# Optimization experiments

Measured on AMD Instinct MI355X. Metric: run time of the kernel, lower is better.

## Reference

```python
import jax, jax.numpy as jnp
import numpy as np

K = 3          # kernel_size
P = 1          # padding
S = 1          # stride
C_IN = 64
C_OUT = 64


def unfold_patches(t, k=K, p=P, s=S):
    """Replicate-pad then extract kxk patches.
    Input  t: [B, C, H, W]
    Output  : [B, Ho, Wo, C, k*k]  matching torch unfold(2).unfold(3).permute(0,2,3,1,4,5).reshape
    (patch index varies as kh*k + kw)."""
    B, C, H, W = t.shape
    tp = jnp.pad(t, ((0, 0), (0, 0), (p, p), (p, p)), mode='edge')
    Ho = (H + 2 * p - k) // s + 1
    Wo = (W + 2 * p - k) // s + 1
    pats = [tp[:, :, a:a + (Ho - 1) * s + 1:s, b:b + (Wo - 1) * s + 1:s]
            for a in range(k) for b in range(k)]
    y = jnp.stack(pats, axis=-1)          # [B, C, Ho, Wo, k*k]
    return jnp.transpose(y, (0, 2, 3, 1, 4))  # [B, Ho, Wo, C, k*k]


def setup_inputs() -> dict:
    key = jax.random.key(0)
    k1, k2, k3, k4, k5, k6, k7 = jax.random.split(key, 7)
    B, H, W = 4, 128, 128
    feat_in = K * K * C_IN * 2      # 1152
    f1_out = K * K * C_IN           # 576
    f2_out = C_IN * C_OUT           # 4096
    lim1 = 1.0 / np.sqrt(feat_in)
    x = jax.random.normal(k1, (B, C_IN, H, W), dtype=jnp.float32)
    m = jax.random.uniform(k2, (B, C_IN, H, W), dtype=jnp.float32)
    s = jax.random.uniform(k3, (B, C_IN, H, W), dtype=jnp.float32)
    W1 = jax.random.uniform(k4, (feat_in, f1_out), minval=-lim1, maxval=lim1, dtype=jnp.float32)
    b1 = jax.random.uniform(k5, (f1_out,), minval=-lim1, maxval=lim1, dtype=jnp.float32)
    W2 = jax.random.uniform(k6, (feat_in, f2_out), minval=-lim1, maxval=lim1, dtype=jnp.float32)
    b2 = jax.random.uniform(k7, (f2_out,), minval=-lim1, maxval=lim1, dtype=jnp.float32)
    return {"x": x, "m": m, "s": s, "W1": W1, "b1": b1, "W2": W2, "b2": b2}


def reference(x, m, s, W1, b1, W2, b2):
    yp = unfold_patches(x)                              # [B,Ho,Wo,Cin,K2]
    mp = jax.lax.stop_gradient(unfold_patches(m))       # torch no_grad
    sp = jax.lax.stop_gradient(unfold_patches(s))
    B, Ho, Wo = yp.shape[:3]

    feat = jnp.concatenate([yp.reshape(B, Ho, Wo, -1),
                            mp.reshape(B, Ho, Wo, -1)], axis=-1)  # [B,Ho,Wo,2*K2*Cin]
    w1 = (feat @ W1 + b1).reshape(B, Ho, Wo, C_IN, K * K)
    w2 = (feat @ W2 + b2).reshape(B, Ho, Wo, C_IN, C_OUT)

    # y = sum_c (sum_k yp*w1) * w2
    yr = jnp.einsum('bhwck,bhwck->bhwc', yp, w1)
    y = jnp.einsum('bhwc,bhwco->bhwo', yr, w2)
    y = jnp.transpose(y, (0, 3, 1, 2))                  # [B,Cout,Ho,Wo]

    aw1 = jnp.abs(w1)
    aw2 = jnp.abs(w2)
    mr = jnp.einsum('bhwck,bhwck->bhwc', mp, aw1)
    m_y = jnp.transpose(jnp.einsum('bhwc,bhwco->bhwo', mr, aw2), (0, 3, 1, 2))
    sr = jnp.einsum('bhwck,bhwck->bhwc', sp, aw1)
    s_y = jnp.transpose(jnp.einsum('bhwc,bhwco->bhwo', sr, aw2), (0, 3, 1, 2))
    m_y = jax.lax.stop_gradient(m_y / s_y)

    return (y, m_y, jnp.ones_like(m_y))
```

## Files before the change

### kernel.cpp

```cpp
#include <hip/hip_runtime.h>
#include <stdint.h>
#include <stddef.h>


using short8   = __attribute__((ext_vector_type(8))) short;
using float4v  = __attribute__((ext_vector_type(4))) float;
using ushort4v = __attribute__((ext_vector_type(4))) unsigned short;

#define DI __device__ __forceinline__

DI unsigned short f2bf(float f) {
  union { float f; unsigned int u; } a; a.f = f;
  unsigned int r = a.u + 0x7fffu + ((a.u >> 16) & 1u);
  return (unsigned short)(r >> 16);
}
DI float bf2f(unsigned short u) {
  union { unsigned int u; float f; } a; a.u = ((unsigned int)u) << 16;
  return a.f;
}
DI void gll16(const void* g, void* l) {
  __builtin_amdgcn_global_load_lds(
      (const __attribute__((address_space(1))) unsigned int*)g,
      (__attribute__((address_space(3))) unsigned int*)l, 16, 0, 0);
}

__global__ void k_feat(const float* __restrict__ x, const float* __restrict__ m,
                       unsigned short* __restrict__ featb) {
  unsigned int v = blockIdx.x * 256u + threadIdx.x;
  unsigned int f = v * 8u;
  int pl   = (f >> 3) & 127;
  int q    = (f >> 10) & 3;
  int pblk = (f >> 12) & 511;
  int kk   = (int)(f >> 21);
  int base = kk * 32 + q * 8;
  const float* src = x;
  int jb = base;
  if (base >= 576) { src = m; jb = base - 576; }
  int p  = pblk * 128 + pl;
  int b  = p >> 14, h = (p >> 7) & 127;
  short8 o;
#pragma unroll
  for (int j = 0; j < 8; ++j) {
    int jx = jb + j;
    int c  = jx / 9;
    int t  = jx - c * 9;
    int t3 = t / 3;
    int dh = t3 - 1;
    int dw = (t - t3 * 3) - 1;
    int hh = min(max(h + dh, 0), 127);
    int ww = min(max(pl + dw, 0), 127);
    o[j] = (short)f2bf(src[(((b << 6) | c) << 14) + (hh << 7) + ww]);
  }
  *(short8*)&featb[(size_t)v * 8] = o;
}

__global__ void k_sw(const float* __restrict__ Wsrc, unsigned short* __restrict__ Wdst,
                     int ncols, int ntiles, int total, int perm) {
  int tid = blockIdx.x * 256 + threadIdx.x;
  if (tid >= total) return;
  int k = tid / ncols;
  int n = tid - k * ncols;
  int np = perm ? (((n & 63) << 6) | (n >> 6)) : n;
  int out = ((k >> 5) * ntiles + (np >> 4)) * 512 + ((k >> 3) & 3) * 128 +
            (np & 15) * 8 + (k & 7);
  Wdst[out] = f2bf(Wsrc[tid]);
}

__launch_bounds__(512, 2)
__global__ void k_gemm1(const unsigned short* __restrict__ featb,
                        const unsigned short* __restrict__ W1s,
                        const float* __restrict__ b1,
                        const float* __restrict__ x, const float* __restrict__ m,
                        const float* __restrict__ s,
                        float* __restrict__ yr, float* __restrict__ mr,
                        float* __restrict__ sr) {
  __shared__ __align__(16) unsigned short Alds[4096];
  __shared__ __align__(16) unsigned short Blds[4608];
  __shared__ __align__(16) unsigned short w1buf[128 * 152];
  const int tid = threadIdx.x;
  const int wv  = tid >> 6;
  const int l15 = tid & 15;
  const int q   = (tid >> 4) & 3;
  const int bm  = blockIdx.x, nb = blockIdx.y;

  float4v acc[9];
#pragma unroll
  for (int t = 0; t < 9; ++t) acc[t] = (float4v){0.f, 0.f, 0.f, 0.f};

  const unsigned short* Ab = featb + (size_t)bm * 4096;
  const unsigned short* Bb = W1s + (size_t)nb * 9 * 512;

  for (int kk = 0; kk < 36; ++kk) {
    __syncthreads();
    gll16(Ab + (size_t)kk * 2097152 + tid * 8, (char*)Alds + wv * 1024);
    gll16(Bb + (size_t)kk * 18432 + tid * 8, (char*)Blds + wv * 1024);
    if (tid < 64) gll16(Bb + (size_t)kk * 18432 + 4096 + tid * 8, (char*)Blds + 8192);
    __syncthreads();
    short8 af = *(const short8*)&Alds[q * 1024 + (16 * wv + l15) * 8];
#pragma unroll
    for (int t = 0; t < 9; ++t) {
      short8 bfr = *(const short8*)&Blds[t * 512 + q * 128 + l15 * 8];
      acc[t] = __builtin_amdgcn_mfma_f32_16x16x32_bf16(af, bfr, acc[t], 0, 0, 0);
    }
  }

#pragma unroll
  for (int t = 0; t < 9; ++t) {
    int col = 16 * t + l15;
    float bb = b1[nb * 144 + col];
#pragma unroll
    for (int i = 0; i < 4; ++i) {
      int plr = 16 * wv + 4 * q + i;
      w1buf[plr * 152 + col] = f2bf(acc[t][i] + bb);
    }
  }
  __syncthreads();

  const int b = bm >> 7, h = bm & 127;
#pragma unroll
  for (int ii = 0; ii < 4; ++ii) {
    int task = ii * 512 + tid;
    int p  = task >> 4;
    int cl = task & 15;
    int c  = nb * 16 + cl;
    float w1v[9];
#pragma unroll
    for (int k = 0; k < 9; ++k) w1v[k] = bf2f(w1buf[p * 152 + cl * 9 + k]);
    size_t base = (size_t)(((b << 6) | c) << 14);
    float vy = 0.f, vm = 0.f, vs = 0.f;
#pragma unroll
    for (int dh = -1; dh <= 1; ++dh) {
      int hh = min(max(h + dh, 0), 127);
#pragma unroll
      for (int dw = -1; dw <= 1; ++dw) {
        int ww = min(max(p + dw, 0), 127);
        size_t idx = base + (hh << 7) + ww;
        int k = (dh + 1) * 3 + (dw + 1);
        float wv1 = w1v[k], aw = fabsf(wv1);
        vy += x[idx] * wv1;
        vm += m[idx] * aw;
        vs += s[idx] * aw;
      }
    }
    size_t P = (size_t)bm * 128 + p;
    yr[P * 64 + c] = vy;
    mr[P * 64 + c] = vm;
    sr[P * 64 + c] = vs;
  }
}

__launch_bounds__(512, 4)
__global__ void k_gemm2(const unsigned short* __restrict__ featb,
                        const unsigned short* __restrict__ W2s,
                        const float* __restrict__ b2,
                        const float* __restrict__ yr, const float* __restrict__ mr,
                        const float* __restrict__ sr,
                        float* __restrict__ out) {
  __shared__ __align__(16) unsigned short U[3][12288];
  unsigned short* w2buf = &U[2][0];
  const int tid  = threadIdx.x;
  const int wv   = tid >> 6;
  const int lane = tid & 63;
  const int wm   = wv >> 2;
  const int wn   = wv & 3;
  const int l15  = tid & 15;
  const int q    = (tid >> 4) & 3;
  const int part = lane >> 4;
  const int bm   = blockIdx.x;
  const int rot  = (bm & 1) * 18;

  const unsigned short* Ab = featb + (size_t)bm * 4096;

  float4v acc[4][4];
#pragma unroll
  for (int r = 0; r < 4; ++r)
#pragma unroll
    for (int t = 0; t < 4; ++t) acc[r][t] = (float4v){0.f, 0.f, 0.f, 0.f};

  {
    int p0 = rot, p1 = rot + 1;
    gll16(Ab + (size_t)p0 * 2097152 + tid * 8, (char*)&U[0][0]    + wv * 1024);
    gll16(W2s + (size_t)p0 * 131072 + tid * 8, (char*)&U[0][4096] + wv * 1024);
    gll16(W2s + (size_t)p0 * 131072 + 4096 + tid * 8, (char*)&U[0][8192] + wv * 1024);
    gll16(Ab + (size_t)p1 * 2097152 + tid * 8, (char*)&U[1][0]    + wv * 1024);
    gll16(W2s + (size_t)p1 * 131072 + tid * 8, (char*)&U[1][4096] + wv * 1024);
    gll16(W2s + (size_t)p1 * 131072 + 4096 + tid * 8, (char*)&U[1][8192] + wv * 1024);
  }

#define G2_KK(KK, BR, BS, DRAIN)                                               \
  do {                                                                         \
    int kks = (KK) + 2, chs = ch;                                              \
    if (kks >= 36) { kks -= 36; chs += 1; }                                    \
    int kkp = kks + rot; if (kkp >= 36) kkp -= 36;          \
    if (DRAIN) { asm volatile("s_waitcnt vmcnt(0)" ::: "memory"); }            \
    else       { asm volatile("s_waitcnt vmcnt(3)" ::: "memory"); }            \
    __builtin_amdgcn_s_barrier();                                              \
    asm volatile("" ::: "memory");                                             \
    if (chs < 16) {                                                            \
      const unsigned short* Ag = Ab + (size_t)kkp * 2097152;                   \
      const unsigned short* Bg = W2s + (size_t)kkp * 131072 + (size_t)chs * 8192; \
      gll16(Ag + tid * 8,        (char*)&U[BS][0]    + wv * 1024);             \
      gll16(Bg + tid * 8,        (char*)&U[BS][4096] + wv * 1024);             \
      gll16(Bg + 4096 + tid * 8, (char*)&U[BS][8192] + wv * 1024);             \
    }                                                                          \
    {                                                                          \
      const unsigned short* Al = &U[BR][0];                                    \
      const unsigned short* Bl = &U[BR][4096];                                 \
      short8 a_[4];                                                            \
      _Pragma("unroll") for (int r = 0; r < 4; ++r)                            \
        a_[r] = *(const short8*)&Al[q * 1024 + (64 * wm + 16 * r + l15) * 8];  \
      __builtin_amdgcn_s_setprio(1);                                           \
      _Pragma("unroll") for (int t = 0; t < 4; ++t) {                          \
        short8 bfr = *(const short8*)&Bl[(4 * wn + t) * 512 + q * 128 + l15 * 8]; \
        _Pragma("unroll") for (int r = 0; r < 4; ++r)                          \
          acc[r][t] = __builtin_amdgcn_mfma_f32_16x16x32_bf16(a_[r], bfr,      \
                                                              acc[r][t], 0, 0, 0); \
      }                                                                        \
      __builtin_amdgcn_s_setprio(0);                                           \
    }                                                                          \
  } while (0)

  for (int ch = 0; ch < 16; ++ch) {
    const bool lc = (ch == 15);
    for (int k3 = 0; k3 < 12; ++k3) {
      const int kk = k3 * 3;
      G2_KK(kk + 0, 0, 2, false);
      G2_KK(kk + 1, 1, 0, (lc && k3 == 11));
      G2_KK(kk + 2, 2, 1, (lc && k3 == 11));
    }

    float b2v[4];
#pragma unroll
    for (int t = 0; t < 4; ++t) b2v[t] = b2[(16 * t + l15) * 64 + 4 * ch + wn];

    for (int p = 0; p < 4; ++p) {
      __syncthreads();
      if (wn == p) {
#pragma unroll
        for (int r = 0; r < 4; ++r)
#pragma unroll
          for (int t = 0; t < 4; ++t)
#pragma unroll
            for (int i = 0; i < 4; ++i)
              w2buf[(64 * wm + 16 * r + 4 * q + i) * 68 + 16 * t + l15] =
                  f2bf(acc[r][t][i] + b2v[t]);
      }
      __syncthreads();
      const int row = 16 * wv + l15;
      const size_t P = (size_t)bm * 128 + row;
      const float4v* y4 = (const float4v*)(yr + P * 64 + 16 * part);
      const float4v* m4 = (const float4v*)(mr + P * 64 + 16 * part);
      const float4v* s4 = (const float4v*)(sr + P * 64 + 16 * part);
      const ushort4v* w4 = (const ushort4v*)&w2buf[row * 68 + 16 * part];
      float ys = 0.f, ms = 0.f, ss = 0.f;
#pragma unroll
      for (int j4 = 0; j4 < 4; ++j4) {
        float4v yv = y4[j4], mv = m4[j4], sv = s4[j4];
        ushort4v wq = w4[j4];
#pragma unroll
        for (int j = 0; j < 4; ++j) {
          float w2f = bf2f(wq[j]);
          float aw  = fabsf(w2f);
          ys += yv[j] * w2f;
          ms += mv[j] * aw;
          ss += sv[j] * aw;
        }
      }
      ys += __shfl_xor(ys, 16); ys += __shfl_xor(ys, 32);
      ms += __shfl_xor(ms, 16); ms += __shfl_xor(ms, 32);
      ss += __shfl_xor(ss, 16); ss += __shfl_xor(ss, 32);
      if (part == 0) {
        const int o = 4 * ch + p;
        const int b = (int)(P >> 14), h = (int)((P >> 7) & 127), w = (int)(P & 127);
        size_t idx = ((size_t)((b << 6) | o) << 14) + (h << 7) + w;
        out[idx]           = ys;
        out[4194304 + idx] = ms / ss;
        out[8388608 + idx] = 1.0f;
      }
    }
#pragma unroll
    for (int r = 0; r < 4; ++r)
#pragma unroll
      for (int t = 0; t < 4; ++t) acc[r][t] = (float4v){0.f, 0.f, 0.f, 0.f};
  }
#undef G2_KK
}

extern "C" void kernel_launch(void* const* d_in, const int* in_sizes, int n_in,
                              void* d_out, int out_size, void* d_ws, size_t ws_size,
                              hipStream_t stream) {
  const float* x  = (const float*)d_in[0];
  const float* m  = (const float*)d_in[1];
  const float* s  = (const float*)d_in[2];
  const float* W1 = (const float*)d_in[3];
  const float* b1 = (const float*)d_in[4];
  const float* W2 = (const float*)d_in[5];
  const float* b2 = (const float*)d_in[6];
  float* out = (float*)d_out;

  if (ws_size < 212090880ull) return;
  char* ws = (char*)d_ws;
  unsigned short* featb = (unsigned short*)ws;
  unsigned short* W1s   = (unsigned short*)(ws + 150994944);
  unsigned short* W2s   = (unsigned short*)(ws + 152322048);
  float* yr = (float*)(ws + 161759232);
  float* mr = (float*)(ws + 178536448);
  float* sr = (float*)(ws + 195313664);

  k_feat<<<36864, 256, 0, stream>>>(x, m, featb);
  k_sw<<<2592, 256, 0, stream>>>(W1, W1s, 576, 36, 663552, 0);
  k_sw<<<18432, 256, 0, stream>>>(W2, W2s, 4096, 256, 4718592, 1);
  dim3 g1(512, 4);
  k_gemm1<<<g1, 512, 0, stream>>>(featb, W1s, b1, x, m, s, yr, mr, sr);
  k_gemm2<<<512, 512, 0, stream>>>(featb, W2s, b2, yr, mr, sr, out);
}
```

Measured before the change: 1.119 ms.

## Triple-buffer gemm1 K-loop with async LDS prefetch and raise occupancy

Replaces gemm1's single-buffered load/sync/compute loop with a three-stage ring of LDS buffers, prefetching two K-steps ahead via global_load_lds and waiting on vmcnt, so that memory latency is overlapped with MFMA work. The epilogue buffer now aliases the ring, which shrinks LDS use and allows launch bounds of 4 blocks per CU. It also removes the per-block rotation of the K start in gemm2, so all blocks walk K in the same order. Risks include register pressure at the higher occupancy and L2 or channel contention from the now-synchronised K order in gemm2.

```diff
diff --git a/kernel.cpp b/kernel.cpp
--- a/kernel.cpp
+++ b/kernel.cpp
@@ -66,7 +66,7 @@
   Wdst[out] = f2bf(Wsrc[tid]);
 }
 
-__launch_bounds__(512, 2)
+__launch_bounds__(512, 4)
 __global__ void k_gemm1(const unsigned short* __restrict__ featb,
                         const unsigned short* __restrict__ W1s,
                         const float* __restrict__ b1,
@@ -74,9 +74,8 @@
                         const float* __restrict__ s,
                         float* __restrict__ yr, float* __restrict__ mr,
                         float* __restrict__ sr) {
-  __shared__ __align__(16) unsigned short Alds[4096];
-  __shared__ __align__(16) unsigned short Blds[4608];
-  __shared__ __align__(16) unsigned short w1buf[128 * 152];
+  __shared__ __align__(16) unsigned short U[3][8704];
+  unsigned short* w1buf = &U[0][0];
   const int tid = threadIdx.x;
   const int wv  = tid >> 6;
   const int l15 = tid & 15;
@@ -90,19 +89,50 @@
   const unsigned short* Ab = featb + (size_t)bm * 4096;
   const unsigned short* Bb = W1s + (size_t)nb * 9 * 512;
 
-  for (int kk = 0; kk < 36; ++kk) {
-    __syncthreads();
-    gll16(Ab + (size_t)kk * 2097152 + tid * 8, (char*)Alds + wv * 1024);
-    gll16(Bb + (size_t)kk * 18432 + tid * 8, (char*)Blds + wv * 1024);
-    if (tid < 64) gll16(Bb + (size_t)kk * 18432 + 4096 + tid * 8, (char*)Blds + 8192);
-    __syncthreads();
-    short8 af = *(const short8*)&Alds[q * 1024 + (16 * wv + l15) * 8];
-#pragma unroll
-    for (int t = 0; t < 9; ++t) {
-      short8 bfr = *(const short8*)&Blds[t * 512 + q * 128 + l15 * 8];
-      acc[t] = __builtin_amdgcn_mfma_f32_16x16x32_bf16(af, bfr, acc[t], 0, 0, 0);
-    }
-  }
+  gll16(Ab + tid * 8, (char*)&U[0][0] + wv * 1024);
+  gll16(Bb + tid * 8, (char*)&U[0][4096] + wv * 1024);
+  if (tid < 64) gll16(Bb + 4096 + tid * 8, (char*)&U[0][8192]);
+  gll16(Ab + 2097152 + tid * 8, (char*)&U[1][0] + wv * 1024);
+  gll16(Bb + 18432 + tid * 8, (char*)&U[1][4096] + wv * 1024);
+  if (tid < 64) gll16(Bb + 18432 + 4096 + tid * 8, (char*)&U[1][8192]);
+
+#define G1_STEP(KK, BR, BS, HEADW)                                             \
+  do {                                                                         \
+    asm volatile("s_waitcnt vmcnt(" #HEADW ")" ::: "memory");                  \
+    __builtin_amdgcn_s_barrier();                                              \
+    asm volatile("" ::: "memory");                                             \
+    {                                                                          \
+      int kks = (KK) + 2;                                                      \
+      if (kks < 36) {                                                          \
+        gll16(Ab + (size_t)kks * 2097152 + tid * 8, (char*)&U[BS][0] + wv * 1024); \
+        gll16(Bb + (size_t)kks * 18432 + tid * 8, (char*)&U[BS][4096] + wv * 1024); \
+        if (tid < 64)                                                          \
+          gll16(Bb + (size_t)kks * 18432 + 4096 + tid * 8, (char*)&U[BS][8192]); \
+      }                                                                        \
+    }                                                                          \
+    {                                                                          \
+      short8 af = *(const short8*)&U[BR][q * 1024 + (16 * wv + l15) * 8];      \
+      __builtin_amdgcn_s_setprio(1);                                           \
+      _Pragma("unroll") for (int t = 0; t < 9; ++t) {                          \
+        short8 bfr = *(const short8*)&U[BR][4096 + t * 512 + q * 128 + l15 * 8]; \
+        acc[t] = __builtin_amdgcn_mfma_f32_16x16x32_bf16(af, bfr, acc[t], 0, 0, 0); \
+      }                                                                        \
+      __builtin_amdgcn_s_setprio(0);                                           \
+    }                                                                          \
+  } while (0)
+
+  for (int k3 = 0; k3 < 11; ++k3) {
+    const int kk = 3 * k3;
+    G1_STEP(kk + 0, 0, 2, 2);
+    G1_STEP(kk + 1, 1, 0, 2);
+    G1_STEP(kk + 2, 2, 1, 2);
+  }
+  G1_STEP(33, 0, 2, 2);
+  G1_STEP(34, 1, 0, 2);
+  G1_STEP(35, 2, 1, 0);
+#undef G1_STEP
+
+  __syncthreads();
 
 #pragma unroll
   for (int t = 0; t < 9; ++t) {
@@ -167,7 +197,6 @@
   const int q    = (tid >> 4) & 3;
   const int part = lane >> 4;
   const int bm   = blockIdx.x;
-  const int rot  = (bm & 1) * 18;
 
   const unsigned short* Ab = featb + (size_t)bm * 4096;
 
@@ -177,28 +206,24 @@
 #pragma unroll
     for (int t = 0; t < 4; ++t) acc[r][t] = (float4v){0.f, 0.f, 0.f, 0.f};
 
-  {
-    int p0 = rot, p1 = rot + 1;
-    gll16(Ab + (size_t)p0 * 2097152 + tid * 8, (char*)&U[0][0]    + wv * 1024);
-    gll16(W2s + (size_t)p0 * 131072 + tid * 8, (char*)&U[0][4096] + wv * 1024);
-    gll16(W2s + (size_t)p0 * 131072 + 4096 + tid * 8, (char*)&U[0][8192] + wv * 1024);
-    gll16(Ab + (size_t)p1 * 2097152 + tid * 8, (char*)&U[1][0]    + wv * 1024);
-    gll16(W2s + (size_t)p1 * 131072 + tid * 8, (char*)&U[1][4096] + wv * 1024);
-    gll16(W2s + (size_t)p1 * 131072 + 4096 + tid * 8, (char*)&U[1][8192] + wv * 1024);
-  }
+  gll16(Ab + tid * 8,                  (char*)&U[0][0]    + wv * 1024);
+  gll16(W2s + tid * 8,                 (char*)&U[0][4096] + wv * 1024);
+  gll16(W2s + 4096 + tid * 8,          (char*)&U[0][8192] + wv * 1024);
+  gll16(Ab + 2097152 + tid * 8,        (char*)&U[1][0]    + wv * 1024);
+  gll16(W2s + 131072 + tid * 8,        (char*)&U[1][4096] + wv * 1024);
+  gll16(W2s + 131072 + 4096 + tid * 8, (char*)&U[1][8192] + wv * 1024);
 
 #define G2_KK(KK, BR, BS, DRAIN)                                               \
   do {                                                                         \
     int kks = (KK) + 2, chs = ch;                                              \
     if (kks >= 36) { kks -= 36; chs += 1; }                                    \
-    int kkp = kks + rot; if (kkp >= 36) kkp -= 36;          \
     if (DRAIN) { asm volatile("s_waitcnt vmcnt(0)" ::: "memory"); }            \
     else       { asm volatile("s_waitcnt vmcnt(3)" ::: "memory"); }            \
     __builtin_amdgcn_s_barrier();                                              \
     asm volatile("" ::: "memory");                                             \
     if (chs < 16) {                                                            \
-      const unsigned short* Ag = Ab + (size_t)kkp * 2097152;                   \
-      const unsigned short* Bg = W2s + (size_t)kkp * 131072 + (size_t)chs * 8192; \
+      const unsigned short* Ag = Ab + (size_t)kks * 2097152;                   \
+      const unsigned short* Bg = W2s + (size_t)kks * 131072 + (size_t)chs * 8192; \
       gll16(Ag + tid * 8,        (char*)&U[BS][0]    + wv * 1024);             \
       gll16(Bg + tid * 8,        (char*)&U[BS][4096] + wv * 1024);             \
       gll16(Bg + 4096 + tid * 8, (char*)&U[BS][8192] + wv * 1024);             \
```

New measurement: 1.181 ms. +5.5%, slower.
